# Kernel optimization log

Hardware: AMD Instinct MI355X
Metric: run time of the kernel (lower is better)

## Reference

```python
import jax, jax.numpy as jnp
import numpy as np

EPSILON = 0.1
ITERATIONS = 100
THRESHOLD = 0.1


def setup_inputs() -> dict:
    key = jax.random.key(0)
    kx, ky = jax.random.split(key)
    x = jax.random.normal(kx, (2048, 64), dtype=jnp.float32)
    y = jax.random.normal(ky, (2048, 64), dtype=jnp.float32)
    return {"x": x, "y": y}


def _sinkhorn(x, y):
    N, M = x.shape[0], y.shape[0]
    # l2 ground metric: C[i,j] = sum_d (x[i,d] - y[j,d])^2   -> [N, M]
    C = jnp.sum((x[:, None, :] - y[None, :, :]) ** 2, axis=-1)
    log_a = jnp.log(1.0 / N + 1e-8)  # uniform marginals (scalar broadcast)
    log_b = jnp.log(1.0 / M + 1e-8)

    def kernel(u, v):
        # log Boltzmann kernel: (-C + u_i + v_j) / epsilon
        return (-C + u[:, None] + v[None, :]) / EPSILON

    def step(carry, _):
        u, v, done = carry
        K = kernel(u, v)
        u_new = EPSILON * (log_a - jax.nn.logsumexp(K, axis=1)) + u
        K2 = kernel(u_new, v)
        # torch: logsumexp(K2.T, dim=1) == logsumexp(K2, axis=0)
        v_new = EPSILON * (log_b - jax.nn.logsumexp(K2, axis=0)) + v
        diff = jnp.sum(jnp.abs(u_new - u)) + jnp.sum(jnp.abs(v_new - v))
        # emulate the host-side early break: freeze state once converged
        u_out = jnp.where(done, u, u_new)
        v_out = jnp.where(done, v, v_new)
        done = done | (diff < THRESHOLD)
        return (u_out, v_out, done), None

    init = (jnp.zeros((N,), C.dtype), jnp.zeros((M,), C.dtype),
            jnp.asarray(False))
    (u, v, _), _ = jax.lax.scan(step, init, None, length=ITERATIONS)

    pi = jnp.exp(kernel(u, v))          # transport plan [N, M]
    cost = jnp.sum(pi * C)              # scalar OT cost
    return cost, pi


def reference(x, y):
    return _sinkhorn(x, y)
```

## Files before the change

kernel.cpp:

```cpp
#include <hip/hip_runtime.h>
#include <cstddef>

static constexpr int   NN      = 2048;
static constexpr int   TPB_B   = 256;
static constexpr int   TPB     = 512;
static constexpr int   NWB     = TPB / 64;
static constexpr int   NB      = 256;
static constexpr int   MAX_IT  = 100;
static constexpr float EPS     = 0.1f;
static constexpr float INV_EPS = 10.0f;
static constexpr float LOG_AB  = -7.6245985063594f;
static constexpr float THRESH  = 0.1f;

#define ALOAD(p)     __hip_atomic_load((p),  __ATOMIC_RELAXED, __HIP_MEMORY_SCOPE_AGENT)
#define ASTORE(p, x) __hip_atomic_store((p), (x), __ATOMIC_RELAXED, __HIP_MEMORY_SCOPE_AGENT)

__global__ __launch_bounds__(TPB_B)
void build_cost(const float* __restrict__ x, const float* __restrict__ y,
                float* __restrict__ C, float* __restrict__ CT,
                float* __restrict__ zz, int c_aligned, int use_ct)
{
    __shared__ float xs[64][65];
    __shared__ float ys[64][65];
    const int t  = threadIdx.x;
    const int bi = blockIdx.y, bj = blockIdx.x;

    if (bi == 0 && bj == 0)
        for (int idx = t; idx < 16384; idx += TPB_B) zz[idx] = 0.0f;

#pragma unroll
    for (int k = 0; k < 16; ++k) {
        int idx = t + TPB_B * k;
        int r = idx >> 6, c = idx & 63;
        xs[r][c] = x[(size_t)(bi * 64 + r) * 64 + c];
        ys[r][c] = y[(size_t)(bj * 64 + r) * 64 + c];
    }
    __syncthreads();

    const int ti0 = (t >> 4) * 4;
    const int tj0 = (t & 15) * 4;
    float acc[4][4] = {};
#pragma unroll 8
    for (int d = 0; d < 64; ++d) {
        float xv[4], yv[4];
#pragma unroll
        for (int k = 0; k < 4; ++k) xv[k] = xs[ti0 + k][d];
#pragma unroll
        for (int l = 0; l < 4; ++l) yv[l] = ys[tj0 + l][d];
#pragma unroll
        for (int k = 0; k < 4; ++k)
#pragma unroll
            for (int l = 0; l < 4; ++l) {
                float df = xv[k] - yv[l];
                acc[k][l] = fmaf(df, df, acc[k][l]);
            }
    }

#pragma unroll
    for (int k = 0; k < 4; ++k) {
        size_t off = (size_t)(bi * 64 + ti0 + k) * NN + bj * 64 + tj0;
        if (c_aligned) {
            *(float4*)(C + off) = make_float4(acc[k][0], acc[k][1], acc[k][2], acc[k][3]);
        } else {
            C[off + 0] = acc[k][0]; C[off + 1] = acc[k][1];
            C[off + 2] = acc[k][2]; C[off + 3] = acc[k][3];
        }
    }
    if (use_ct) {
#pragma unroll
        for (int l = 0; l < 4; ++l) {
            size_t off = (size_t)(bj * 64 + tj0 + l) * NN + bi * 64 + ti0;
            *(float4*)(CT + off) = make_float4(acc[0][l], acc[1][l], acc[2][l], acc[3][l]);
        }
    }
}

__device__ __forceinline__ void load_row32(const float* row, int lane,
                                           int aligned, float c[32])
{
    if (aligned) {
        const float4* r4 = (const float4*)row;
#pragma unroll
        for (int k = 0; k < 8; ++k) {
            float4 A = r4[lane + 64 * k];
            c[4*k+0] = A.x; c[4*k+1] = A.y; c[4*k+2] = A.z; c[4*k+3] = A.w;
        }
    } else {
#pragma unroll
        for (int k = 0; k < 8; ++k) {
            const float* p = row + 4 * (lane + 64 * k);
            c[4*k+0] = p[0]; c[4*k+1] = p[1]; c[4*k+2] = p[2]; c[4*k+3] = p[3];
        }
    }
}

__device__ __forceinline__ void lds_row32(const float* sv, int lane, float b[32])
{
    const float4* s4 = (const float4*)sv;
#pragma unroll
    for (int k = 0; k < 8; ++k) {
        float4 A = s4[lane + 64 * k];
        b[4*k+0] = A.x; b[4*k+1] = A.y; b[4*k+2] = A.z; b[4*k+3] = A.w;
    }
}

__device__ __forceinline__ float wave_lse(const float c[32], const float b[32])
{
    float M = b[0] - c[0];
#pragma unroll
    for (int k = 1; k < 32; ++k) M = fmaxf(M, b[k] - c[k]);
#pragma unroll
    for (int off = 1; off < 64; off <<= 1) M = fmaxf(M, __shfl_xor(M, off));
    float Ms = M * INV_EPS;
    float s = 0.0f;
#pragma unroll
    for (int k = 0; k < 32; ++k) s += __expf(fmaf(b[k] - c[k], INV_EPS, -Ms));
#pragma unroll
    for (int off = 1; off < 64; off <<= 1) s += __shfl_xor(s, off);
    return Ms + __logf(s);
}

__global__ __launch_bounds__(TPB)
void sinkhorn_main(const float* Cm, const float* __restrict__ CT,
                   unsigned long long* __restrict__ valA,
                   unsigned long long* __restrict__ valB,
                   unsigned long long* __restrict__ rotR,
                   unsigned long long* __restrict__ rotC,
                   unsigned long long* __restrict__ costb,
                   float* out, int c_aligned, int use_ct)
{
    __shared__ float sv[2048];
    __shared__ float swave[NWB];
    __shared__ float sdw[NWB];
    __shared__ float sred4[4];
    __shared__ float sdiff;
    const int t = threadIdx.x, lane = t & 63, w = t >> 6, b = blockIdx.x;
    const int i = b * NWB + w;

    float crow[32], ccol[32];
    load_row32(Cm + (size_t)i * NN, lane, c_aligned, crow);
    if (use_ct) {
        load_row32(CT + (size_t)i * NN, lane, 1, ccol);
    } else {
#pragma unroll
        for (int k = 0; k < 8; ++k)
#pragma unroll
            for (int kk = 0; kk < 4; ++kk)
                ccol[4*k+kk] = Cm[(size_t)(4 * (lane + 64 * k) + kk) * NN + i];
    }

    for (int k = t; k < 2048; k += TPB) sv[k] = 0.0f;
    __syncthreads();

    float u_keep = 0.0f, v_keep = 0.0f;
    float b32[32];

    for (int it = 0; it < MAX_IT; ++it) {
        const unsigned ep = (unsigned)(it + 1);

        lds_row32(sv, lane, b32);
        float lse   = wave_lse(crow, b32);
        float u_new = EPS * (LOG_AB - lse);
        float pdr   = fabsf(u_new - u_keep);

        if (it >= 1) {
            if (t < 256) {
                unsigned long long r1, r2;
                const int ri = (it & 3) * 256 + t;
                for (;;) { r1 = ALOAD(&rotR[ri]);
                           if ((unsigned)(r1 >> 32) >= (unsigned)it) break; }
                for (;;) { r2 = ALOAD(&rotC[ri]);
                           if ((unsigned)(r2 >> 32) >= (unsigned)it) break; }
                float d = __uint_as_float((unsigned)r1) +
                          __uint_as_float((unsigned)r2);
#pragma unroll
                for (int off = 1; off < 64; off <<= 1) d += __shfl_xor(d, off);
                if (lane == 0) sred4[w] = d;
            }
            __syncthreads();
            if (t == 0) sdiff = sred4[0] + sred4[1] + sred4[2] + sred4[3];
            __syncthreads();
            if (sdiff < THRESH) break;
        }
        u_keep = u_new;

        if (lane == 0) { swave[w] = u_new; sdw[w] = pdr; }
        __syncthreads();
        if (t < NWB)
            ASTORE(&valA[b * NWB + t],
                   ((unsigned long long)ep << 32) | __float_as_uint(swave[t]));
        if (t == 0) {
            float ps = 0.0f;
#pragma unroll
            for (int k = 0; k < NWB; ++k) ps += sdw[k];
            ASTORE(&rotR[(ep & 3) * 256 + b],
                   ((unsigned long long)ep << 32) | __float_as_uint(ps));
        }
        {
            unsigned long long d0, d1, d2, d3;
            const int base = 4 * t;
            for (;;) {
                d0 = ALOAD(&valA[base + 0]); d1 = ALOAD(&valA[base + 1]);
                d2 = ALOAD(&valA[base + 2]); d3 = ALOAD(&valA[base + 3]);
                bool ok = ((unsigned)(d0 >> 32) >= ep) & ((unsigned)(d1 >> 32) >= ep)
                        & ((unsigned)(d2 >> 32) >= ep) & ((unsigned)(d3 >> 32) >= ep);
                if (ok) break;
            }
            ((float4*)sv)[t] = make_float4(__uint_as_float((unsigned)d0),
                                           __uint_as_float((unsigned)d1),
                                           __uint_as_float((unsigned)d2),
                                           __uint_as_float((unsigned)d3));
        }
        __syncthreads();

        lds_row32(sv, lane, b32);
        lse = wave_lse(ccol, b32);
        float v_new = EPS * (LOG_AB - lse);
        float pdc   = fabsf(v_new - v_keep);
        v_keep = v_new;

        if (lane == 0) { swave[w] = v_new; sdw[w] = pdc; }
        __syncthreads();
        if (t < NWB)
            ASTORE(&valB[b * NWB + t],
                   ((unsigned long long)ep << 32) | __float_as_uint(swave[t]));
        if (t == 0) {
            float ps = 0.0f;
#pragma unroll
            for (int k = 0; k < NWB; ++k) ps += sdw[k];
            ASTORE(&rotC[(ep & 3) * 256 + b],
                   ((unsigned long long)ep << 32) | __float_as_uint(ps));
        }
        {
            unsigned long long d0, d1, d2, d3;
            const int base = 4 * t;
            for (;;) {
                d0 = ALOAD(&valB[base + 0]); d1 = ALOAD(&valB[base + 1]);
                d2 = ALOAD(&valB[base + 2]); d3 = ALOAD(&valB[base + 3]);
                bool ok = ((unsigned)(d0 >> 32) >= ep) & ((unsigned)(d1 >> 32) >= ep)
                        & ((unsigned)(d2 >> 32) >= ep) & ((unsigned)(d3 >> 32) >= ep);
                if (ok) break;
            }
            ((float4*)sv)[t] = make_float4(__uint_as_float((unsigned)d0),
                                           __uint_as_float((unsigned)d1),
                                           __uint_as_float((unsigned)d2),
                                           __uint_as_float((unsigned)d3));
        }
        __syncthreads();
    }

    float cpart = 0.0f;
    {
        lds_row32(sv, lane, b32);
        const float ui = u_keep;
        float* orow = out + 1 + (size_t)i * NN;
#pragma unroll
        for (int k = 0; k < 8; ++k) {
#pragma unroll
            for (int kk = 0; kk < 4; ++kk) {
                float cc = crow[4*k+kk];
                float p  = __expf((ui + b32[4*k+kk] - cc) * INV_EPS);
                cpart = fmaf(p, cc, cpart);
                orow[4 * (lane + 64 * k) + kk] = p;
            }
        }
    }
#pragma unroll
    for (int off = 1; off < 64; off <<= 1) cpart += __shfl_xor(cpart, off);
    if (lane == 0) sdw[w] = cpart;
    __syncthreads();
    if (t == 0) {
        float pc = 0.0f;
#pragma unroll
        for (int k = 0; k < NWB; ++k) pc += sdw[k];
        ASTORE(&costb[b], (1ull << 32) | __float_as_uint(pc));
    }
    if (b == 0) {
        if (t < 256) {
            unsigned long long h;
            for (;;) { h = ALOAD(&costb[t]); if ((unsigned)(h >> 32) >= 1u) break; }
            float pc = __uint_as_float((unsigned)h);
#pragma unroll
            for (int off = 1; off < 64; off <<= 1) pc += __shfl_xor(pc, off);
            if (lane == 0) sred4[w] = pc;
        }
        __syncthreads();
        if (t == 0) out[0] = sred4[0] + sred4[1] + sred4[2] + sred4[3];
    }
}

extern "C" void kernel_launch(void* const* d_in, const int* in_sizes, int n_in,
                              void* d_out, int out_size, void* d_ws, size_t ws_size,
                              hipStream_t stream)
{
    (void)in_sizes; (void)n_in; (void)out_size;
    const float* x = (const float*)d_in[0];
    const float* y = (const float*)d_in[1];
    float* out = (float*)d_out;
    char*  ws  = (char*)d_ws;

    const size_t CB = (size_t)NN * NN * sizeof(float);
    const size_t ZZ = 128 * 1024;

    float *Cm, *CT, *zz;
    int c_aligned, use_ct;
    if (ws_size >= 2 * CB + ZZ) {
        Cm = (float*)ws; CT = (float*)(ws + CB); zz = (float*)(ws + 2 * CB);
        c_aligned = 1; use_ct = 1;
    } else if (ws_size >= CB + ZZ) {
        Cm = out + 1; CT = (float*)ws; zz = (float*)(ws + CB);
        c_aligned = 0; use_ct = 1;
    } else {
        Cm = out + 1; CT = nullptr; zz = (float*)ws;
        c_aligned = 0; use_ct = 0;
    }
    unsigned long long* zz64  = (unsigned long long*)zz;
    unsigned long long* valA  = zz64;
    unsigned long long* valB  = zz64 + 2048;
    unsigned long long* rotR  = zz64 + 4096;
    unsigned long long* rotC  = zz64 + 5120;
    unsigned long long* costb = zz64 + 6144;

    hipLaunchKernelGGL(build_cost, dim3(32, 32), dim3(TPB_B), 0, stream,
                       x, y, Cm, CT, zz, c_aligned, use_ct);

    const float* Cmc = Cm;
    const float* CTc = CT;
    void* args[] = { (void*)&Cmc, (void*)&CTc, (void*)&valA, (void*)&valB,
                     (void*)&rotR, (void*)&rotC, (void*)&costb,
                     (void*)&out, (void*)&c_aligned, (void*)&use_ct };
    hipLaunchCooperativeKernel((void*)sinkhorn_main, dim3(NB), dim3(TPB),
                               args, 0, stream);
}
```

Measured before the change: 827.1 us.

## Replicate cross-block exchange buffers and compute convergence locally from gathered vectors

Each block now writes its u/v values into G replicated copies of the exchange array, and every block polls only its own replica. This spreads polling traffic across more cache lines and reduces contention. The separate per-block diff rotation buffers are dropped: each block computes the L1 change itself from the full old and new u/v vectors kept in two LDS arrays, which removes one spin-wait phase per iteration. The zeroing of the now-larger flag area is spread across 32 blocks of the cost build. The cost is more atomic stores per block and more workspace.

Result: slower. 1.206 ms (+45.8%).

```diff
diff --git a/kernel.cpp b/kernel.cpp
--- a/kernel.cpp
+++ b/kernel.cpp
@@ -15,18 +15,25 @@
 #define ALOAD(p)     __hip_atomic_load((p),  __ATOMIC_RELAXED, __HIP_MEMORY_SCOPE_AGENT)
 #define ASTORE(p, x) __hip_atomic_store((p), (x), __ATOMIC_RELAXED, __HIP_MEMORY_SCOPE_AGENT)
 
+typedef unsigned long long u64;
+
 __global__ __launch_bounds__(TPB_B)
 void build_cost(const float* __restrict__ x, const float* __restrict__ y,
                 float* __restrict__ C, float* __restrict__ CT,
-                float* __restrict__ zz, int c_aligned, int use_ct)
+                unsigned* __restrict__ zz, int zcount,
+                int c_aligned, int use_ct)
 {
     __shared__ float xs[64][65];
     __shared__ float ys[64][65];
     const int t  = threadIdx.x;
     const int bi = blockIdx.y, bj = blockIdx.x;
 
-    if (bi == 0 && bj == 0)
-        for (int idx = t; idx < 16384; idx += TPB_B) zz[idx] = 0.0f;
+    if (bi == 0) {
+        int per = (zcount + 31) / 32;
+        int lo = bj * per;
+        int hi = lo + per; if (hi > zcount) hi = zcount;
+        for (int idx = lo + t; idx < hi; idx += TPB_B) zz[idx] = 0u;
+    }
 
 #pragma unroll
     for (int k = 0; k < 16; ++k) {
@@ -120,22 +127,49 @@
     return Ms + __logf(s);
 }
 
+__device__ __forceinline__ void poll_deposit(const u64* rep, unsigned ep,
+                                             float* dst, float* pdw, int t)
+{
+    const int lane = t & 63, w = t >> 6;
+    const int base = 4 * t;
+    u64 d0, d1, d2, d3;
+    for (;;) {
+        d0 = ALOAD(rep + base + 0); d1 = ALOAD(rep + base + 1);
+        d2 = ALOAD(rep + base + 2); d3 = ALOAD(rep + base + 3);
+        bool ok = ((unsigned)(d0 >> 32) >= ep) & ((unsigned)(d1 >> 32) >= ep)
+                & ((unsigned)(d2 >> 32) >= ep) & ((unsigned)(d3 >> 32) >= ep);
+        if (ok) break;
+    }
+    float n0 = __uint_as_float((unsigned)d0);
+    float n1 = __uint_as_float((unsigned)d1);
+    float n2 = __uint_as_float((unsigned)d2);
+    float n3 = __uint_as_float((unsigned)d3);
+    float4 o = ((float4*)dst)[t];
+    float du = fabsf(n0 - o.x) + fabsf(n1 - o.y) + fabsf(n2 - o.z) + fabsf(n3 - o.w);
+    ((float4*)dst)[t] = make_float4(n0, n1, n2, n3);
+#pragma unroll
+    for (int off = 1; off < 64; off <<= 1) du += __shfl_xor(du, off);
+    if (lane == 0) pdw[w] = du;
+}
+
 __global__ __launch_bounds__(TPB)
 void sinkhorn_main(const float* Cm, const float* __restrict__ CT,
-                   unsigned long long* __restrict__ valA,
-                   unsigned long long* __restrict__ valB,
-                   unsigned long long* __restrict__ rotR,
-                   unsigned long long* __restrict__ rotC,
-                   unsigned long long* __restrict__ costb,
-                   float* out, int c_aligned, int use_ct)
-{
-    __shared__ float sv[2048];
+                   u64* __restrict__ repA, u64* __restrict__ repB,
+                   u64* __restrict__ costb,
+                   float* out, int c_aligned, int use_ct,
+                   int gmask, int gshift)
+{
+    __shared__ float su[2048];
+    __shared__ float svv[2048];
     __shared__ float swave[NWB];
-    __shared__ float sdw[NWB];
+    __shared__ float sdu[NWB];
+    __shared__ float sdv[NWB];
     __shared__ float sred4[4];
     __shared__ float sdiff;
     const int t = threadIdx.x, lane = t & 63, w = t >> 6, b = blockIdx.x;
     const int i = b * NWB + w;
+    const u64* myA = repA + ((size_t)(b & gmask)) * 2048;
+    const u64* myB = repB + ((size_t)(b & gmask)) * 2048;
 
     float crow[32], ccol[32];
     load_row32(Cm + (size_t)i * NN, lane, c_aligned, crow);
@@ -149,109 +183,58 @@
                 ccol[4*k+kk] = Cm[(size_t)(4 * (lane + 64 * k) + kk) * NN + i];
     }
 
-    for (int k = t; k < 2048; k += TPB) sv[k] = 0.0f;
+    for (int k = t; k < 2048; k += TPB) { su[k] = 0.0f; svv[k] = 0.0f; }
     __syncthreads();
 
-    float u_keep = 0.0f, v_keep = 0.0f;
+    float u_keep = 0.0f;
     float b32[32];
+    const int nposts = 8 << gshift;
 
     for (int it = 0; it < MAX_IT; ++it) {
         const unsigned ep = (unsigned)(it + 1);
 
-        lds_row32(sv, lane, b32);
+        if (it >= 1) {
+            if (t == 0) {
+                float s = 0.0f;
+#pragma unroll
+                for (int k = 0; k < NWB; ++k) s += sdu[k];
+#pragma unroll
+                for (int k = 0; k < NWB; ++k) s += sdv[k];
+                sdiff = s;
+            }
+            __syncthreads();
+            if (sdiff < THRESH) break;
+        }
+
+        lds_row32(svv, lane, b32);
         float lse   = wave_lse(crow, b32);
         float u_new = EPS * (LOG_AB - lse);
-        float pdr   = fabsf(u_new - u_keep);
-
-        if (it >= 1) {
-            if (t < 256) {
-                unsigned long long r1, r2;
-                const int ri = (it & 3) * 256 + t;
-                for (;;) { r1 = ALOAD(&rotR[ri]);
-                           if ((unsigned)(r1 >> 32) >= (unsigned)it) break; }
-                for (;;) { r2 = ALOAD(&rotC[ri]);
-                           if ((unsigned)(r2 >> 32) >= (unsigned)it) break; }
-                float d = __uint_as_float((unsigned)r1) +
-                          __uint_as_float((unsigned)r2);
-#pragma unroll
-                for (int off = 1; off < 64; off <<= 1) d += __shfl_xor(d, off);
-                if (lane == 0) sred4[w] = d;
-            }
-            __syncthreads();
-            if (t == 0) sdiff = sred4[0] + sred4[1] + sred4[2] + sred4[3];
-            __syncthreads();
-            if (sdiff < THRESH) break;
-        }
+        if (lane == 0) swave[w] = u_new;
+        __syncthreads();
+
+        if (t < nposts)
+            ASTORE(&repA[((size_t)(t & gmask)) * 2048 + b * NWB + (t >> gshift)],
+                   ((u64)ep << 32) | __float_as_uint(swave[t >> gshift]));
+        poll_deposit(myA, ep, su, sdu, t);
         u_keep = u_new;
-
-        if (lane == 0) { swave[w] = u_new; sdw[w] = pdr; }
-        __syncthreads();
-        if (t < NWB)
-            ASTORE(&valA[b * NWB + t],
-                   ((unsigned long long)ep << 32) | __float_as_uint(swave[t]));
-        if (t == 0) {
-            float ps = 0.0f;
-#pragma unroll
-            for (int k = 0; k < NWB; ++k) ps += sdw[k];
-            ASTORE(&rotR[(ep & 3) * 256 + b],
-                   ((unsigned long long)ep << 32) | __float_as_uint(ps));
-        }
-        {
-            unsigned long long d0, d1, d2, d3;
-            const int base = 4 * t;
-            for (;;) {
-                d0 = ALOAD(&valA[base + 0]); d1 = ALOAD(&valA[base + 1]);
-                d2 = ALOAD(&valA[base + 2]); d3 = ALOAD(&valA[base + 3]);
-                bool ok = ((unsigned)(d0 >> 32) >= ep) & ((unsigned)(d1 >> 32) >= ep)
-                        & ((unsigned)(d2 >> 32) >= ep) & ((unsigned)(d3 >> 32) >= ep);
-                if (ok) break;
-            }
-            ((float4*)sv)[t] = make_float4(__uint_as_float((unsigned)d0),
-                                           __uint_as_float((unsigned)d1),
-                                           __uint_as_float((unsigned)d2),
-                                           __uint_as_float((unsigned)d3));
-        }
-        __syncthreads();
-
-        lds_row32(sv, lane, b32);
+        __syncthreads();
+
+        lds_row32(su, lane, b32);
         lse = wave_lse(ccol, b32);
         float v_new = EPS * (LOG_AB - lse);
-        float pdc   = fabsf(v_new - v_keep);
-        v_keep = v_new;
-
-        if (lane == 0) { swave[w] = v_new; sdw[w] = pdc; }
-        __syncthreads();
-        if (t < NWB)
-            ASTORE(&valB[b * NWB + t],
-                   ((unsigned long long)ep << 32) | __float_as_uint(swave[t]));
-        if (t == 0) {
-            float ps = 0.0f;
-#pragma unroll
-            for (int k = 0; k < NWB; ++k) ps += sdw[k];
-            ASTORE(&rotC[(ep & 3) * 256 + b],
-                   ((unsigned long long)ep << 32) | __float_as_uint(ps));
-        }
-        {
-            unsigned long long d0, d1, d2, d3;
-            const int base = 4 * t;
-            for (;;) {
-                d0 = ALOAD(&valB[base + 0]); d1 = ALOAD(&valB[base + 1]);
-                d2 = ALOAD(&valB[base + 2]); d3 = ALOAD(&valB[base + 3]);
-                bool ok = ((unsigned)(d0 >> 32) >= ep) & ((unsigned)(d1 >> 32) >= ep)
-                        & ((unsigned)(d2 >> 32) >= ep) & ((unsigned)(d3 >> 32) >= ep);
-                if (ok) break;
-            }
-            ((float4*)sv)[t] = make_float4(__uint_as_float((unsigned)d0),
-                                           __uint_as_float((unsigned)d1),
-                                           __uint_as_float((unsigned)d2),
-                                           __uint_as_float((unsigned)d3));
-        }
+        if (lane == 0) swave[w] = v_new;
+        __syncthreads();
+
+        if (t < nposts)
+            ASTORE(&repB[((size_t)(t & gmask)) * 2048 + b * NWB + (t >> gshift)],
+                   ((u64)ep << 32) | __float_as_uint(swave[t >> gshift]));
+        poll_deposit(myB, ep, svv, sdv, t);
         __syncthreads();
     }
 
     float cpart = 0.0f;
     {
-        lds_row32(sv, lane, b32);
+        lds_row32(svv, lane, b32);
         const float ui = u_keep;
         float* orow = out + 1 + (size_t)i * NN;
 #pragma unroll
@@ -267,17 +250,17 @@
     }
 #pragma unroll
     for (int off = 1; off < 64; off <<= 1) cpart += __shfl_xor(cpart, off);
-    if (lane == 0) sdw[w] = cpart;
+    if (lane == 0) sdu[w] = cpart;
     __syncthreads();
     if (t == 0) {
         float pc = 0.0f;
 #pragma unroll
-        for (int k = 0; k < NWB; ++k) pc += sdw[k];
+        for (int k = 0; k < NWB; ++k) pc += sdu[k];
         ASTORE(&costb[b], (1ull << 32) | __float_as_uint(pc));
     }
     if (b == 0) {
         if (t < 256) {
-            unsigned long long h;
+            u64 h;
             for (;;) { h = ALOAD(&costb[t]); if ((unsigned)(h >> 32) >= 1u) break; }
             float pc = __uint_as_float((unsigned)h);
 #pragma unroll
@@ -300,35 +283,42 @@
     char*  ws  = (char*)d_ws;
 
     const size_t CB = (size_t)NN * NN * sizeof(float);
-    const size_t ZZ = 128 * 1024;
-
-    float *Cm, *CT, *zz;
-    int c_aligned, use_ct;
-    if (ws_size >= 2 * CB + ZZ) {
-        Cm = (float*)ws; CT = (float*)(ws + CB); zz = (float*)(ws + 2 * CB);
-        c_aligned = 1; use_ct = 1;
-    } else if (ws_size >= CB + ZZ) {
-        Cm = out + 1; CT = (float*)ws; zz = (float*)(ws + CB);
-        c_aligned = 0; use_ct = 1;
+    auto zbytes = [](int G) -> size_t { return ((size_t)G * 4096 + 256) * 8; };
+
+    float *Cm, *CT; char* zz;
+    int c_aligned, use_ct, G;
+    if (ws_size >= 2 * CB + zbytes(32)) {
+        Cm = (float*)ws; CT = (float*)(ws + CB); zz = ws + 2 * CB;
+        c_aligned = 1; use_ct = 1; G = 32;
+    } else if (ws_size >= CB + zbytes(32)) {
+        Cm = out + 1; CT = (float*)ws; zz = ws + CB;
+        c_aligned = 0; use_ct = 1; G = 32;
+    } else if (ws_size >= CB + zbytes(4)) {
+        Cm = out + 1; CT = (float*)ws; zz = ws + CB;
+        c_aligned = 0; use_ct = 1; G = 4;
+    } else if (ws_size >= zbytes(4)) {
+        Cm = out + 1; CT = nullptr; zz = ws;
+        c_aligned = 0; use_ct = 0; G = 4;
     } else {
-        Cm = out + 1; CT = nullptr; zz = (float*)ws;
-        c_aligned = 0; use_ct = 0;
-    }
-    unsigned long long* zz64  = (unsigned long long*)zz;
-    unsigned long long* valA  = zz64;
-    unsigned long long* valB  = zz64 + 2048;
-    unsigned long long* rotR  = zz64 + 4096;
-    unsigned long long* rotC  = zz64 + 5120;
-    unsigned long long* costb = zz64 + 6144;
+        Cm = out + 1; CT = nullptr; zz = ws;
+        c_aligned = 0; use_ct = 0; G = 1;
+    }
+    int gmask = G - 1;
+    int gshift = (G == 32) ? 5 : (G == 4) ? 2 : 0;
+
+    u64* repA  = (u64*)zz;
+    u64* repB  = repA + (size_t)G * 2048;
+    u64* costb = repB + (size_t)G * 2048;
+    int  zcount = (G * 4096 + 256) * 2;
 
     hipLaunchKernelGGL(build_cost, dim3(32, 32), dim3(TPB_B), 0, stream,
-                       x, y, Cm, CT, zz, c_aligned, use_ct);
+                       x, y, Cm, CT, (unsigned*)zz, zcount, c_aligned, use_ct);
 
     const float* Cmc = Cm;
     const float* CTc = CT;
-    void* args[] = { (void*)&Cmc, (void*)&CTc, (void*)&valA, (void*)&valB,
-                     (void*)&rotR, (void*)&rotC, (void*)&costb,
-                     (void*)&out, (void*)&c_aligned, (void*)&use_ct };
+    void* args[] = { (void*)&Cmc, (void*)&CTc, (void*)&repA, (void*)&repB,
+                     (void*)&costb, (void*)&out, (void*)&c_aligned,
+                     (void*)&use_ct, (void*)&gmask, (void*)&gshift };
     hipLaunchCooperativeKernel((void*)sinkhorn_main, dim3(NB), dim3(TPB),
                                args, 0, stream);
 }
```

## Halve cooperative grid to 128 blocks of 1024 threads and spread flag zeroing

Applied to the files above, without the earlier changes.

Switches the persistent cooperative Sinkhorn kernel from 256 blocks of 512 threads to 128 blocks of 1024 threads. Each block still owns 16 rows, so the grid-wide flag-polling barriers (valA/valB gathers and rotation diffs) have half as many producers. Each thread now polls two flags instead of four. The zeroing of the sync workspace is shrunk to the size actually used and split across the 32 first-row blocks of build_cost instead of one block. The change uses fewer CUs and packs more waves per block, which may reduce latency hiding and raise register pressure under the 1024-thread launch bound.

Result: faster. 737.6 us (median of 2 runs) (-10.8%).

```diff
diff --git a/kernel.cpp b/kernel.cpp
--- a/kernel.cpp
+++ b/kernel.cpp
@@ -3,9 +3,9 @@
 
 static constexpr int   NN      = 2048;
 static constexpr int   TPB_B   = 256;
-static constexpr int   TPB     = 512;
+static constexpr int   TPB     = 1024;
 static constexpr int   NWB     = TPB / 64;
-static constexpr int   NB      = 256;
+static constexpr int   NB      = 128;
 static constexpr int   MAX_IT  = 100;
 static constexpr float EPS     = 0.1f;
 static constexpr float INV_EPS = 10.0f;
@@ -15,18 +15,25 @@
 #define ALOAD(p)     __hip_atomic_load((p),  __ATOMIC_RELAXED, __HIP_MEMORY_SCOPE_AGENT)
 #define ASTORE(p, x) __hip_atomic_store((p), (x), __ATOMIC_RELAXED, __HIP_MEMORY_SCOPE_AGENT)
 
+typedef unsigned long long u64;
+
 __global__ __launch_bounds__(TPB_B)
 void build_cost(const float* __restrict__ x, const float* __restrict__ y,
                 float* __restrict__ C, float* __restrict__ CT,
-                float* __restrict__ zz, int c_aligned, int use_ct)
+                unsigned* __restrict__ zz, int zcount,
+                int c_aligned, int use_ct)
 {
     __shared__ float xs[64][65];
     __shared__ float ys[64][65];
     const int t  = threadIdx.x;
     const int bi = blockIdx.y, bj = blockIdx.x;
 
-    if (bi == 0 && bj == 0)
-        for (int idx = t; idx < 16384; idx += TPB_B) zz[idx] = 0.0f;
+    if (bi == 0) {
+        int per = (zcount + 31) / 32;
+        int lo = bj * per;
+        int hi = lo + per; if (hi > zcount) hi = zcount;
+        for (int idx = lo + t; idx < hi; idx += TPB_B) zz[idx] = 0u;
+    }
 
 #pragma unroll
     for (int k = 0; k < 16; ++k) {
@@ -122,11 +129,9 @@
 
 __global__ __launch_bounds__(TPB)
 void sinkhorn_main(const float* Cm, const float* __restrict__ CT,
-                   unsigned long long* __restrict__ valA,
-                   unsigned long long* __restrict__ valB,
-                   unsigned long long* __restrict__ rotR,
-                   unsigned long long* __restrict__ rotC,
-                   unsigned long long* __restrict__ costb,
+                   u64* __restrict__ valA, u64* __restrict__ valB,
+                   u64* __restrict__ rotR, u64* __restrict__ rotC,
+                   u64* __restrict__ costb,
                    float* out, int c_aligned, int use_ct)
 {
     __shared__ float sv[2048];
@@ -164,9 +169,9 @@
         float pdr   = fabsf(u_new - u_keep);
 
         if (it >= 1) {
-            if (t < 256) {
-                unsigned long long r1, r2;
-                const int ri = (it & 3) * 256 + t;
+            if (t < NB) {
+                u64 r1, r2;
+                const int ri = (it & 3) * NB + t;
                 for (;;) { r1 = ALOAD(&rotR[ri]);
                            if ((unsigned)(r1 >> 32) >= (unsigned)it) break; }
                 for (;;) { r2 = ALOAD(&rotC[ri]);
@@ -178,7 +183,7 @@
                 if (lane == 0) sred4[w] = d;
             }
             __syncthreads();
-            if (t == 0) sdiff = sred4[0] + sred4[1] + sred4[2] + sred4[3];
+            if (t == 0) sdiff = sred4[0] + sred4[1];
             __syncthreads();
             if (sdiff < THRESH) break;
         }
@@ -188,28 +193,25 @@
         __syncthreads();
         if (t < NWB)
             ASTORE(&valA[b * NWB + t],
-                   ((unsigned long long)ep << 32) | __float_as_uint(swave[t]));
+                   ((u64)ep << 32) | __float_as_uint(swave[t]));
         if (t == 0) {
             float ps = 0.0f;
 #pragma unroll
             for (int k = 0; k < NWB; ++k) ps += sdw[k];
-            ASTORE(&rotR[(ep & 3) * 256 + b],
-                   ((unsigned long long)ep << 32) | __float_as_uint(ps));
+            ASTORE(&rotR[(ep & 3) * NB + b],
+                   ((u64)ep << 32) | __float_as_uint(ps));
         }
         {
-            unsigned long long d0, d1, d2, d3;
-            const int base = 4 * t;
+            const int base = 2 * t;
+            u64 d0, d1;
             for (;;) {
-                d0 = ALOAD(&valA[base + 0]); d1 = ALOAD(&valA[base + 1]);
-                d2 = ALOAD(&valA[base + 2]); d3 = ALOAD(&valA[base + 3]);
-                bool ok = ((unsigned)(d0 >> 32) >= ep) & ((unsigned)(d1 >> 32) >= ep)
-                        & ((unsigned)(d2 >> 32) >= ep) & ((unsigned)(d3 >> 32) >= ep);
-                if (ok) break;
-            }
-            ((float4*)sv)[t] = make_float4(__uint_as_float((unsigned)d0),
-                                           __uint_as_float((unsigned)d1),
-                                           __uint_as_float((unsigned)d2),
-                                           __uint_as_float((unsigned)d3));
+                d0 = ALOAD(&valA[base + 0]);
+                d1 = ALOAD(&valA[base + 1]);
+                if (((unsigned)(d0 >> 32) >= ep) & ((unsigned)(d1 >> 32) >= ep))
+                    break;
+            }
+            ((float2*)sv)[t] = make_float2(__uint_as_float((unsigned)d0),
+                                           __uint_as_float((unsigned)d1));
         }
         __syncthreads();
 
@@ -223,28 +225,25 @@
         __syncthreads();
         if (t < NWB)
             ASTORE(&valB[b * NWB + t],
-                   ((unsigned long long)ep << 32) | __float_as_uint(swave[t]));
+                   ((u64)ep << 32) | __float_as_uint(swave[t]));
         if (t == 0) {
             float ps = 0.0f;
 #pragma unroll
             for (int k = 0; k < NWB; ++k) ps += sdw[k];
-            ASTORE(&rotC[(ep & 3) * 256 + b],
-                   ((unsigned long long)ep << 32) | __float_as_uint(ps));
+            ASTORE(&rotC[(ep & 3) * NB + b],
+                   ((u64)ep << 32) | __float_as_uint(ps));
         }
         {
-            unsigned long long d0, d1, d2, d3;
-            const int base = 4 * t;
+            const int base = 2 * t;
+            u64 d0, d1;
             for (;;) {
-                d0 = ALOAD(&valB[base + 0]); d1 = ALOAD(&valB[base + 1]);
-                d2 = ALOAD(&valB[base + 2]); d3 = ALOAD(&valB[base + 3]);
-                bool ok = ((unsigned)(d0 >> 32) >= ep) & ((unsigned)(d1 >> 32) >= ep)
-                        & ((unsigned)(d2 >> 32) >= ep) & ((unsigned)(d3 >> 32) >= ep);
-                if (ok) break;
-            }
-            ((float4*)sv)[t] = make_float4(__uint_as_float((unsigned)d0),
-                                           __uint_as_float((unsigned)d1),
-                                           __uint_as_float((unsigned)d2),
-                                           __uint_as_float((unsigned)d3));
+                d0 = ALOAD(&valB[base + 0]);
+                d1 = ALOAD(&valB[base + 1]);
+                if (((unsigned)(d0 >> 32) >= ep) & ((unsigned)(d1 >> 32) >= ep))
+                    break;
+            }
+            ((float2*)sv)[t] = make_float2(__uint_as_float((unsigned)d0),
+                                           __uint_as_float((unsigned)d1));
         }
         __syncthreads();
     }
@@ -276,16 +275,16 @@
         ASTORE(&costb[b], (1ull << 32) | __float_as_uint(pc));
     }
     if (b == 0) {
-        if (t < 256) {
-            unsigned long long h;
-            for (;;) { h = ALOAD(&costb[t]); if ((unsigned)(h >> 32) >= 1u) break; }
+        if (t < NB) {
+            u64 h;
+            for (;;) { h = ALOAD(&costb[t]); if (h >= (1ull << 32)) break; }
             float pc = __uint_as_float((unsigned)h);
 #pragma unroll
             for (int off = 1; off < 64; off <<= 1) pc += __shfl_xor(pc, off);
             if (lane == 0) sred4[w] = pc;
         }
         __syncthreads();
-        if (t == 0) out[0] = sred4[0] + sred4[1] + sred4[2] + sred4[3];
+        if (t == 0) out[0] = sred4[0] + sred4[1];
     }
 }
 
@@ -300,29 +299,30 @@
     char*  ws  = (char*)d_ws;
 
     const size_t CB = (size_t)NN * NN * sizeof(float);
-    const size_t ZZ = 128 * 1024;
-
-    float *Cm, *CT, *zz;
+    const int    ZU = 2048 + 2048 + 512 + 512 + 128;
+    const size_t ZB = (size_t)ZU * sizeof(u64);
+
+    float *Cm, *CT; char* zz;
     int c_aligned, use_ct;
-    if (ws_size >= 2 * CB + ZZ) {
-        Cm = (float*)ws; CT = (float*)(ws + CB); zz = (float*)(ws + 2 * CB);
+    if (ws_size >= 2 * CB + ZB) {
+        Cm = (float*)ws; CT = (float*)(ws + CB); zz = ws + 2 * CB;
         c_aligned = 1; use_ct = 1;
-    } else if (ws_size >= CB + ZZ) {
-        Cm = out + 1; CT = (float*)ws; zz = (float*)(ws + CB);
+    } else if (ws_size >= CB + ZB) {
+        Cm = out + 1; CT = (float*)ws; zz = ws + CB;
         c_aligned = 0; use_ct = 1;
     } else {
-        Cm = out + 1; CT = nullptr; zz = (float*)ws;
+        Cm = out + 1; CT = nullptr; zz = ws;
         c_aligned = 0; use_ct = 0;
     }
-    unsigned long long* zz64  = (unsigned long long*)zz;
-    unsigned long long* valA  = zz64;
-    unsigned long long* valB  = zz64 + 2048;
-    unsigned long long* rotR  = zz64 + 4096;
-    unsigned long long* rotC  = zz64 + 5120;
-    unsigned long long* costb = zz64 + 6144;
+    u64* valA  = (u64*)zz;
+    u64* valB  = valA + 2048;
+    u64* rotR  = valB + 2048;
+    u64* rotC  = rotR + 512;
+    u64* costb = rotC + 512;
+    int  zcount = ZU * 2;
 
     hipLaunchKernelGGL(build_cost, dim3(32, 32), dim3(TPB_B), 0, stream,
-                       x, y, Cm, CT, zz, c_aligned, use_ct);
+                       x, y, Cm, CT, (unsigned*)zz, zcount, c_aligned, use_ct);
 
     const float* Cmc = Cm;
     const float* CTc = CT;
```
